# Optimization experiments

Hardware: AMD Instinct MI355X
Metric: run time of the kernel (lower is better)

## Reference

```python
import jax, jax.numpy as jnp
import numpy as np

N = 100000   # nodes
E = 1600000  # edges
B = 64       # graphs
F = 16       # node features
H = 128      # hidden dim
G = 8        # graph features
C = 2        # classes
NGIN = 2     # extra GIN layers after the first
BN_EPS = 1e-5


def elu01(x):
    # F.elu with alpha=0.1
    return jnp.where(x > 0, x, 0.1 * jnp.expm1(x))


def batchnorm(h, gamma, beta):
    # training-mode BatchNorm1d: biased batch statistics
    mu = h.mean(axis=0)
    var = h.var(axis=0)
    return (h - mu) * jax.lax.rsqrt(var + BN_EPS) * gamma + beta


def gin_layer(x, src, dst, W1, b1, gm, bt, W2, b2):
    # GINConv eps=0: MLP(x + sum_{j->i} x_j), then ELU(0.1)
    agg = jax.ops.segment_sum(x[src], dst, num_segments=x.shape[0])
    h = (x + agg) @ W1 + b1
    h = jax.nn.relu(batchnorm(h, gm, bt))
    return elu01(h @ W2 + b2)


def setup_inputs() -> dict:
    key = jax.random.key(0)
    ks = jax.random.split(key, 24)
    s = 0.05
    inp = {
        "h0": jax.random.normal(ks[0], (N, F), jnp.float32),
        "coord0": jax.random.normal(ks[1], (N, 3), jnp.float32),
        "g0": jax.random.normal(ks[2], (B, G), jnp.float32),
        "edge_index": jax.random.randint(ks[3], (2, E), 0, N, jnp.int32),
        "batch": jnp.sort(jax.random.randint(ks[4], (N,), 0, B, jnp.int32)),
        # first GIN layer: (F+3) -> H -> H
        "w1_0": jax.random.normal(ks[5], (F + 3, H), jnp.float32) * s,
        "b1_0": jnp.zeros((H,), jnp.float32),
        "gm_0": jnp.ones((H,), jnp.float32),
        "bt_0": jnp.zeros((H,), jnp.float32),
        "w2_0": jax.random.normal(ks[6], (H, H), jnp.float32) * s,
        "b2_0": jnp.zeros((H,), jnp.float32),
        # NGIN stacked layers: H -> H -> H
        "w1_r": jax.random.normal(ks[7], (NGIN, H, H), jnp.float32) * s,
        "b1_r": jnp.zeros((NGIN, H), jnp.float32),
        "gm_r": jnp.ones((NGIN, H), jnp.float32),
        "bt_r": jnp.zeros((NGIN, H), jnp.float32),
        "w2_r": jax.random.normal(ks[8], (NGIN, H, H), jnp.float32) * s,
        "b2_r": jnp.zeros((NGIN, H), jnp.float32),
        # classifier: (2H+G) -> H -> C
        "cw1": jax.random.normal(ks[9], (2 * H + G, H), jnp.float32) * s,
        "cb1": jnp.zeros((H,), jnp.float32),
        "cgm": jnp.ones((H,), jnp.float32),
        "cbt": jnp.zeros((H,), jnp.float32),
        "cw2": jax.random.normal(ks[10], (H, C), jnp.float32) * s,
        "cb2": jnp.zeros((C,), jnp.float32),
    }
    return inp


def reference(h0, coord0, g0, edge_index, batch,
              w1_0, b1_0, gm_0, bt_0, w2_0, b2_0,
              w1_r, b1_r, gm_r, bt_r, w2_r, b2_r,
              cw1, cb1, cgm, cbt, cw2, cb2):
    src, dst = edge_index[0], edge_index[1]
    x = jnp.concatenate([h0, coord0], axis=1)  # [N, F+3]
    x = gin_layer(x, src, dst, w1_0, b1_0, gm_0, bt_0, w2_0, b2_0)
    for i in range(NGIN):
        x = gin_layer(x, src, dst, w1_r[i], b1_r[i], gm_r[i], bt_r[i], w2_r[i], b2_r[i])
    # global mean + max pooling per graph
    nb = g0.shape[0]
    cnt = jax.ops.segment_sum(jnp.ones((x.shape[0], 1), x.dtype), batch, num_segments=nb)
    mean_p = jax.ops.segment_sum(x, batch, num_segments=nb) / jnp.maximum(cnt, 1.0)
    max_p = jax.ops.segment_max(x, batch, num_segments=nb)
    pooled = jnp.concatenate([mean_p, max_p], axis=-1)  # [B, 2H]
    z = jnp.concatenate([pooled, g0], axis=1)           # [B, 2H+G]
    z = elu01(z @ cw1 + cb1)
    z = batchnorm(z, cgm, cbt)
    logits = z @ cw2 + cb2
    return jax.nn.softmax(logits, axis=1)
```

## Files before the change

### kernel.cpp

```cpp
#include <hip/hip_runtime.h>
#include <math.h>

#define NN 100000
#define EE 1600000
#define BB 64
#define FF 16
#define HH 128
#define GG 8
#define K0 19
#define BN_EPS 1e-5f
#define PCH 16
#define BSHIFT 8
#define BNODES 256
#define NBINS 391
#define BCAP 8192
#define ACH 2048
#define NB_WP 320
#define NB_X0 12500
#define STSLOT 8

typedef short bf16x8 __attribute__((ext_vector_type(8)));
typedef float f32x4 __attribute__((ext_vector_type(4)));

__device__ __forceinline__ float elu01f(float v) {
    return v > 0.f ? v : 0.1f * (__expf(v) - 1.f);
}

__device__ __forceinline__ unsigned f2bfu(float f) {
    unsigned u = __float_as_uint(f);
    unsigned r = u + 0x7FFFu + ((u >> 16) & 1u);
    return r >> 16;
}
__device__ __forceinline__ short f2bf(float f) { return (short)f2bfu(f); }
__device__ __forceinline__ float bfu2f(unsigned short b) {
    return __uint_as_float(((unsigned)b) << 16);
}
__device__ __forceinline__ float bflo(unsigned u) { return __uint_as_float(u << 16); }
__device__ __forceinline__ float bfhi(unsigned u) { return __uint_as_float(u & 0xffff0000u); }

__global__ __launch_bounds__(512) void k_binA(const int* __restrict__ esrc, const int* __restrict__ edst,
                                              int* __restrict__ bincnt, uint2* __restrict__ binbuf) {
    __shared__ int hist[NBINS];
    __shared__ int gbase[NBINS];
    __shared__ int cur[NBINS];
    __shared__ int sc[512];
    __shared__ uint2 ebuf[ACH];
    __shared__ uint2 sorted[ACH];
    int tid = threadIdx.x;
    int e0 = blockIdx.x * ACH;
    int n = min(ACH, EE - e0);
    if (tid < NBINS) hist[tid] = 0;
    __syncthreads();
    for (int i = tid; i < n; i += 512) {
        int s = esrc[e0 + i];
        int d = edst[e0 + i];
        ebuf[i] = make_uint2((unsigned)s, (unsigned)d);
        atomicAdd(&hist[d >> BSHIFT], 1);
    }
    __syncthreads();
    sc[tid] = (tid < NBINS) ? hist[tid] : 0;
    __syncthreads();
    for (int off = 1; off < 512; off <<= 1) {
        int v = (tid >= off) ? sc[tid - off] : 0;
        __syncthreads();
        sc[tid] += v;
        __syncthreads();
    }
    if (tid < NBINS) {
        int c = hist[tid];
        gbase[tid] = (c > 0) ? atomicAdd(&bincnt[tid], c) : 0;
        cur[tid] = (tid > 0) ? sc[tid - 1] : 0;
    }
    __syncthreads();
    for (int i = tid; i < n; i += 512) {
        uint2 e = ebuf[i];
        int b = (int)(e.y >> BSHIFT);
        int pos = atomicAdd(&cur[b], 1);
        sorted[pos] = e;
    }
    __syncthreads();
    for (int i = tid; i < n; i += 512) {
        uint2 e = sorted[i];
        int b = (int)(e.y >> BSHIFT);
        int ls = (b > 0) ? sc[b - 1] : 0;
        int gpos = gbase[b] + (i - ls);
        binbuf[(size_t)b * BCAP + gpos] = e;
    }
}

__global__ __launch_bounds__(512) void k_binB(const uint2* __restrict__ binbuf, const int* __restrict__ bincnt,
                                              int* __restrict__ rp, int* __restrict__ srcs) {
    __shared__ int hist[BNODES];
    __shared__ int scx[BNODES];
    __shared__ int scur[BNODES];
    __shared__ int rsum[512];
    __shared__ int sbuf[BCAP];
    int b = blockIdx.x;
    int n = bincnt[b];
    int tid = threadIdx.x;
    rsum[tid] = (tid < b) ? bincnt[tid] : 0;
    if (tid < BNODES) hist[tid] = 0;
    __syncthreads();
    for (int off = 256; off > 0; off >>= 1) {
        if (tid < off) rsum[tid] += rsum[tid + off];
        __syncthreads();
    }
    int base = rsum[0];
    const uint2* eb = binbuf + (size_t)b * BCAP;
    for (int i = tid; i < n; i += 512)
        atomicAdd(&hist[eb[i].y & (BNODES - 1)], 1);
    __syncthreads();
    if (tid < BNODES) scx[tid] = hist[tid];
    __syncthreads();
    for (int off = 1; off < BNODES; off <<= 1) {
        int vv = (tid >= off && tid < BNODES) ? scx[tid - off] : 0;
        __syncthreads();
        if (tid < BNODES) scx[tid] += vv;
        __syncthreads();
    }
    if (tid < BNODES) {
        int excl = (tid > 0) ? scx[tid - 1] : 0;
        int node = (b << BSHIFT) + tid;
        if (node < NN) rp[node] = base + excl;
        scur[tid] = excl;
    }
    if (b == NBINS - 1 && tid == 0) rp[NN] = EE;
    __syncthreads();
    for (int i = tid; i < n; i += 512) {
        uint2 e = eb[i];
        int pos = atomicAdd(&scur[e.y & (BNODES - 1)], 1);
        sbuf[pos] = (int)e.x;
    }
    __syncthreads();
    for (int i = tid; i < n; i += 512) srcs[base + i] = sbuf[i];
}

__global__ __launch_bounds__(256) void k_prep(const float* __restrict__ w2_0, const float* __restrict__ w1_r,
                                              const float* __restrict__ w2_r, short* __restrict__ wt,
                                              const float* __restrict__ h0, const float* __restrict__ coord,
                                              unsigned short* __restrict__ x0,
                                              const int* __restrict__ batch, int* __restrict__ gptr) {
    int b = blockIdx.x;
    int tid = threadIdx.x;
    if (b == 0 && tid <= BB) {
        int t = tid;
        int lo = 0, hi = NN;
        while (lo < hi) { int mid = (lo + hi) >> 1; if (batch[mid] < t) lo = mid + 1; else hi = mid; }
        gptr[t] = lo;
    }
    if (b < NB_WP) {
        int t = b * 256 + tid;
        if (t >= 5 * HH * HH) return;
        int m = t >> 14;
        int rem = t & 16383;
        int col = rem >> 7;
        int k = rem & 127;
        const float* src = (m == 0) ? w2_0 : (m <= 2 ? w1_r + (size_t)(m - 1) * HH * HH
                                                     : w2_r + (size_t)(m - 3) * HH * HH);
        wt[t] = f2bf(src[k * HH + col]);
    } else {
        int i = (b - NB_WP) * 256 + tid;
        if (i >= NN * 32) return;
        int node = i >> 5, k = i & 31;
        float v = 0.f;
        if (k < FF) v = h0[node * FF + k];
        else if (k < K0) v = coord[node * 3 + (k - FF)];
        x0[i] = (unsigned short)f2bfu(v);
    }
}

__global__ __launch_bounds__(256) void k_agg_small(const uint4* __restrict__ x, const int* __restrict__ rp,
                                                   const int* __restrict__ srcs, float* __restrict__ y) {
    int w = (blockIdx.x * 256 + threadIdx.x) >> 6;
    int lane = threadIdx.x & 63;
    if (w >= NN) return;
    int e = lane >> 2, q = lane & 3;
    int beg = rp[w], end = rp[w + 1];
    float acc[8];
    {
        if (e == 0) {
            uint4 u = x[(size_t)w * 4 + q];
            acc[0] = bflo(u.x); acc[1] = bfhi(u.x);
            acc[2] = bflo(u.y); acc[3] = bfhi(u.y);
            acc[4] = bflo(u.z); acc[5] = bfhi(u.z);
            acc[6] = bflo(u.w); acc[7] = bfhi(u.w);
        } else {
            #pragma unroll
            for (int j = 0; j < 8; j++) acc[j] = 0.f;
        }
    }
    for (int p = beg; p < end; p += 16) {
        int rem = end - p;
        bool act = e < rem;
        int sn = act ? srcs[p + e] : 0;
        uint4 u = x[(size_t)sn * 4 + q];
        float m = act ? 1.f : 0.f;
        acc[0] = fmaf(m, bflo(u.x), acc[0]); acc[1] = fmaf(m, bfhi(u.x), acc[1]);
        acc[2] = fmaf(m, bflo(u.y), acc[2]); acc[3] = fmaf(m, bfhi(u.y), acc[3]);
        acc[4] = fmaf(m, bflo(u.z), acc[4]); acc[5] = fmaf(m, bfhi(u.z), acc[5]);
        acc[6] = fmaf(m, bflo(u.w), acc[6]); acc[7] = fmaf(m, bfhi(u.w), acc[7]);
    }
    #pragma unroll
    for (int mask = 4; mask <= 32; mask <<= 1)
        #pragma unroll
        for (int j = 0; j < 8; j++)
            acc[j] += __shfl_xor(acc[j], mask, 64);
    if (e == 0) {
        float4* yo = (float4*)(y + (size_t)w * 32 + q * 8);
        yo[0] = make_float4(acc[0], acc[1], acc[2], acc[3]);
        yo[1] = make_float4(acc[4], acc[5], acc[6], acc[7]);
    }
}

template<int K>
__global__ __launch_bounds__(256) void k_gemm_small(const float* __restrict__ in,
        const float* __restrict__ W, const float* __restrict__ bias,
        unsigned short* __restrict__ out, float* __restrict__ gstat) {
    constexpr int SK = ((K + 3) / 4) * 4 + 4;
    __shared__ __align__(16) float yt[32 * SK];
    __shared__ float red[256];
    int tid = threadIdx.x;
    int row0 = blockIdx.x * 32;
    for (int t = tid; t < 32 * SK; t += 256) {
        int r = t / SK, k = t - r * SK;
        float v = 0.f;
        if (k < K) v = in[(size_t)(row0 + r) * 32 + k];
        yt[t] = v;
    }
    __syncthreads();
    int col = tid & 127;
    int rg = tid >> 7;
    float acc[16];
    #pragma unroll
    for (int r = 0; r < 16; r++) acc[r] = 0.f;
    const float* ybase = &yt[rg * 16 * SK];
    int kk = 0;
    for (; kk + 4 <= K; kk += 4) {
        float w0 = W[(kk + 0) * HH + col];
        float w1 = W[(kk + 1) * HH + col];
        float w2 = W[(kk + 2) * HH + col];
        float w3 = W[(kk + 3) * HH + col];
        #pragma unroll
        for (int r = 0; r < 16; r++) {
            const float4 v = *(const float4*)&ybase[r * SK + kk];
            acc[r] = fmaf(v.x, w0, acc[r]);
            acc[r] = fmaf(v.y, w1, acc[r]);
            acc[r] = fmaf(v.z, w2, acc[r]);
            acc[r] = fmaf(v.w, w3, acc[r]);
        }
    }
    if constexpr (K % 4 != 0) {
        float w[4];
        #pragma unroll
        for (int j = 0; j < 4; j++) w[j] = (kk + j < K) ? W[(kk + j) * HH + col] : 0.f;
        #pragma unroll
        for (int r = 0; r < 16; r++) {
            const float4 v = *(const float4*)&ybase[r * SK + kk];
            acc[r] = fmaf(v.x, w[0], acc[r]);
            acc[r] = fmaf(v.y, w[1], acc[r]);
            acc[r] = fmaf(v.z, w[2], acc[r]);
            acc[r] = fmaf(v.w, w[3], acc[r]);
        }
    }
    float bcol = bias[col];
    float s = 0.f, s2 = 0.f;
    #pragma unroll
    for (int r = 0; r < 16; r++) {
        float hv = acc[r] + bcol;
        out[(size_t)(row0 + rg * 16 + r) * HH + col] = (unsigned short)f2bfu(hv);
        s += hv; s2 = fmaf(hv, hv, s2);
    }
    int sl = (blockIdx.x & (STSLOT - 1)) << 8;
    red[tid] = s; __syncthreads();
    if (tid < 128) atomicAdd(&gstat[sl + tid], s + red[tid + 128]);
    __syncthreads();
    red[tid] = s2; __syncthreads();
    if (tid < 128) atomicAdd(&gstat[sl + 128 + tid], s2 + red[tid + 128]);
}

__global__ __launch_bounds__(256) void k_agg128_bf(const uint4* __restrict__ x4, const int* __restrict__ rp,
                                                   const int* __restrict__ srcs, uint4* __restrict__ y4) {
    int wave = (blockIdx.x * 256 + threadIdx.x) >> 6;
    int lane = threadIdx.x & 63;
    int g = lane >> 4, il = lane & 15;
    int w = wave * 4 + g;
    if (w >= NN) return;
    int beg = rp[w], end = rp[w + 1];
    uint4 u = x4[(size_t)w * 16 + il];
    float a0 = bflo(u.x), a1 = bfhi(u.x), a2 = bflo(u.y), a3 = bfhi(u.y);
    float a4 = bflo(u.z), a5 = bfhi(u.z), a6 = bflo(u.w), a7 = bfhi(u.w);
    float b0 = 0.f, b1 = 0.f, b2 = 0.f, b3 = 0.f, b4 = 0.f, b5 = 0.f, b6 = 0.f, b7 = 0.f;
    int p = beg;
    for (; p + 8 <= end; p += 8) {
        int s0 = srcs[p + 0], s1 = srcs[p + 1], s2 = srcs[p + 2], s3 = srcs[p + 3];
        int s4 = srcs[p + 4], s5 = srcs[p + 5], s6 = srcs[p + 6], s7 = srcs[p + 7];
        uint4 u0 = x4[(size_t)s0 * 16 + il];
        uint4 u1 = x4[(size_t)s1 * 16 + il];
        uint4 u2 = x4[(size_t)s2 * 16 + il];
        uint4 u3 = x4[(size_t)s3 * 16 + il];
        uint4 u4 = x4[(size_t)s4 * 16 + il];
        uint4 u5 = x4[(size_t)s5 * 16 + il];
        uint4 u6 = x4[(size_t)s6 * 16 + il];
        uint4 u7 = x4[(size_t)s7 * 16 + il];
        a0 += (bflo(u0.x) + bflo(u1.x)) + (bflo(u2.x) + bflo(u3.x));
        a1 += (bfhi(u0.x) + bfhi(u1.x)) + (bfhi(u2.x) + bfhi(u3.x));
        a2 += (bflo(u0.y) + bflo(u1.y)) + (bflo(u2.y) + bflo(u3.y));
        a3 += (bfhi(u0.y) + bfhi(u1.y)) + (bfhi(u2.y) + bfhi(u3.y));
        a4 += (bflo(u0.z) + bflo(u1.z)) + (bflo(u2.z) + bflo(u3.z));
        a5 += (bfhi(u0.z) + bfhi(u1.z)) + (bfhi(u2.z) + bfhi(u3.z));
        a6 += (bflo(u0.w) + bflo(u1.w)) + (bflo(u2.w) + bflo(u3.w));
        a7 += (bfhi(u0.w) + bfhi(u1.w)) + (bfhi(u2.w) + bfhi(u3.w));
        b0 += (bflo(u4.x) + bflo(u5.x)) + (bflo(u6.x) + bflo(u7.x));
        b1 += (bfhi(u4.x) + bfhi(u5.x)) + (bfhi(u6.x) + bfhi(u7.x));
        b2 += (bflo(u4.y) + bflo(u5.y)) + (bflo(u6.y) + bflo(u7.y));
        b3 += (bfhi(u4.y) + bfhi(u5.y)) + (bfhi(u6.y) + bfhi(u7.y));
        b4 += (bflo(u4.z) + bflo(u5.z)) + (bflo(u6.z) + bflo(u7.z));
        b5 += (bfhi(u4.z) + bfhi(u5.z)) + (bfhi(u6.z) + bfhi(u7.z));
        b6 += (bflo(u4.w) + bflo(u5.w)) + (bflo(u6.w) + bflo(u7.w));
        b7 += (bfhi(u4.w) + bfhi(u5.w)) + (bfhi(u6.w) + bfhi(u7.w));
    }
    for (; p + 4 <= end; p += 4) {
        int s0 = srcs[p + 0], s1 = srcs[p + 1], s2 = srcs[p + 2], s3 = srcs[p + 3];
        uint4 u0 = x4[(size_t)s0 * 16 + il];
        uint4 u1 = x4[(size_t)s1 * 16 + il];
        uint4 u2 = x4[(size_t)s2 * 16 + il];
        uint4 u3 = x4[(size_t)s3 * 16 + il];
        a0 += (bflo(u0.x) + bflo(u1.x)) + (bflo(u2.x) + bflo(u3.x));
        a1 += (bfhi(u0.x) + bfhi(u1.x)) + (bfhi(u2.x) + bfhi(u3.x));
        a2 += (bflo(u0.y) + bflo(u1.y)) + (bflo(u2.y) + bflo(u3.y));
        a3 += (bfhi(u0.y) + bfhi(u1.y)) + (bfhi(u2.y) + bfhi(u3.y));
        a4 += (bflo(u0.z) + bflo(u1.z)) + (bflo(u2.z) + bflo(u3.z));
        a5 += (bfhi(u0.z) + bfhi(u1.z)) + (bfhi(u2.z) + bfhi(u3.z));
        a6 += (bflo(u0.w) + bflo(u1.w)) + (bflo(u2.w) + bflo(u3.w));
        a7 += (bfhi(u0.w) + bfhi(u1.w)) + (bfhi(u2.w) + bfhi(u3.w));
    }
    for (; p < end; ++p) {
        uint4 uu = x4[(size_t)srcs[p] * 16 + il];
        a0 += bflo(uu.x); a1 += bfhi(uu.x);
        a2 += bflo(uu.y); a3 += bfhi(uu.y);
        a4 += bflo(uu.z); a5 += bfhi(uu.z);
        a6 += bflo(uu.w); a7 += bfhi(uu.w);
    }
    a0 += b0; a1 += b1; a2 += b2; a3 += b3;
    a4 += b4; a5 += b5; a6 += b6; a7 += b7;
    uint4 o;
    o.x = f2bfu(a0) | (f2bfu(a1) << 16);
    o.y = f2bfu(a2) | (f2bfu(a3) << 16);
    o.z = f2bfu(a4) | (f2bfu(a5) << 16);
    o.w = f2bfu(a6) | (f2bfu(a7) << 16);
    y4[(size_t)w * 16 + il] = o;
}

__global__ __launch_bounds__(256) void k_gemm_s1(const unsigned short* __restrict__ in,
        const short* __restrict__ WT, const float* __restrict__ bias,
        unsigned short* __restrict__ out, float* __restrict__ gstat) {
    __shared__ __align__(16) short Al[64 * 136];
    __shared__ float lsum[HH], lsq[HH];
    int tid = threadIdx.x;
    if (tid < HH) { lsum[tid] = 0.f; lsq[tid] = 0.f; }
    int row0 = blockIdx.x * 64;
    {
        int r = tid >> 2;
        int k0 = (tid & 3) * 32;
        int grow = row0 + r;
        uint4* d4 = (uint4*)&Al[r * 136 + k0];
        if (grow < NN) {
            const uint4* s4 = (const uint4*)(in + (size_t)grow * HH + k0);
            d4[0] = s4[0]; d4[1] = s4[1]; d4[2] = s4[2]; d4[3] = s4[3];
        } else {
            uint4 z = {0, 0, 0, 0};
            d4[0] = z; d4[1] = z; d4[2] = z; d4[3] = z;
        }
    }
    __syncthreads();
    int wave = tid >> 6;
    int lane = tid & 63;
    int ln = lane & 15, quad = lane >> 4;
    int wcol0 = wave * 32;
    f32x4 acc[4][2];
    #pragma unroll
    for (int rt = 0; rt < 4; rt++)
        #pragma unroll
        for (int ct = 0; ct < 2; ct++) acc[rt][ct] = (f32x4){0.f, 0.f, 0.f, 0.f};
    #pragma unroll
    for (int ks = 0; ks < 4; ks++) {
        bf16x8 a[4], b[2];
        #pragma unroll
        for (int ct = 0; ct < 2; ct++)
            b[ct] = *(const bf16x8*)(WT + (size_t)(wcol0 + ct * 16 + ln) * HH + ks * 32 + quad * 8);
        #pragma unroll
        for (int rt = 0; rt < 4; rt++)
            a[rt] = *(const bf16x8*)(&Al[(rt * 16 + ln) * 136 + ks * 32 + quad * 8]);
        #pragma unroll
        for (int rt = 0; rt < 4; rt++)
            #pragma unroll
            for (int ct = 0; ct < 2; ct++)
                acc[rt][ct] = __builtin_amdgcn_mfma_f32_16x16x32_bf16(a[rt], b[ct], acc[rt][ct], 0, 0, 0);
    }
    float b0 = bias[wcol0 + ln];
    float b1 = bias[wcol0 + 16 + ln];
    float s[2] = {0.f, 0.f}, s2[2] = {0.f, 0.f};
    #pragma unroll
    for (int rt = 0; rt < 4; rt++) {
        #pragma unroll
        for (int r = 0; r < 4; r++) {
            int grow = row0 + rt * 16 + quad * 4 + r;
            if (grow < NN) {
                float hv0 = acc[rt][0][r] + b0;
                float hv1 = acc[rt][1][r] + b1;
                out[(size_t)grow * HH + wcol0 + ln] = (unsigned short)f2bfu(hv0);
                out[(size_t)grow * HH + wcol0 + 16 + ln] = (unsigned short)f2bfu(hv1);
                s[0] += hv0; s2[0] = fmaf(hv0, hv0, s2[0]);
                s[1] += hv1; s2[1] = fmaf(hv1, hv1, s2[1]);
            }
        }
    }
    atomicAdd(&lsum[wcol0 + ln], s[0]);
    atomicAdd(&lsum[wcol0 + 16 + ln], s[1]);
    atomicAdd(&lsq[wcol0 + ln], s2[0]);
    atomicAdd(&lsq[wcol0 + 16 + ln], s2[1]);
    __syncthreads();
    if (tid < HH) {
        int sl = (blockIdx.x & (STSLOT - 1)) << 8;
        atomicAdd(&gstat[sl + tid], lsum[tid]);
        atomicAdd(&gstat[sl + 128 + tid], lsq[tid]);
    }
}

__global__ __launch_bounds__(256) void k_gemm_bn(const unsigned short* __restrict__ in,
        const short* __restrict__ WT, const float* __restrict__ bias,
        const float* __restrict__ gstat, const float* __restrict__ gm, const float* __restrict__ bt,
        unsigned short* __restrict__ out) {
    __shared__ __align__(16) short Al[64 * 136];
    __shared__ __align__(16) float bnsc[HH], bnsh[HH];
    int tid = threadIdx.x;
    if (tid < HH) {
        float s = 0.f, s2 = 0.f;
        #pragma unroll
        for (int k = 0; k < STSLOT; ++k) {
            s += gstat[(k << 8) + tid];
            s2 += gstat[(k << 8) + 128 + tid];
        }
        float mu = s * (1.f / NN);
        float var = fmaxf(s2 * (1.f / NN) - mu * mu, 0.f);
        float a = gm[tid] * rsqrtf(var + BN_EPS);
        bnsc[tid] = a;
        bnsh[tid] = fmaf(-mu, a, bt[tid]);
    }
    __syncthreads();
    int row0 = blockIdx.x * 64;
    {
        int r = tid >> 2;
        int k0 = (tid & 3) * 32;
        int grow = row0 + r;
        short* dst = &Al[r * 136 + k0];
        if (grow < NN) {
            const uint4* s4 = (const uint4*)(in + (size_t)grow * HH + k0);
            unsigned* d = (unsigned*)dst;
            #pragma unroll
            for (int q = 0; q < 4; q++) {
                uint4 u = s4[q];
                float4 sc0 = *(const float4*)(bnsc + k0 + q * 8);
                float4 sh0 = *(const float4*)(bnsh + k0 + q * 8);
                float4 sc1 = *(const float4*)(bnsc + k0 + q * 8 + 4);
                float4 sh1 = *(const float4*)(bnsh + k0 + q * 8 + 4);
                float a0 = bflo(u.x), a1 = bfhi(u.x);
                float a2 = bflo(u.y), a3 = bfhi(u.y);
                float a4 = bflo(u.z), a5 = bfhi(u.z);
                float a6 = bflo(u.w), a7 = bfhi(u.w);
                a0 = fmaxf(fmaf(a0, sc0.x, sh0.x), 0.f);
                a1 = fmaxf(fmaf(a1, sc0.y, sh0.y), 0.f);
                a2 = fmaxf(fmaf(a2, sc0.z, sh0.z), 0.f);
                a3 = fmaxf(fmaf(a3, sc0.w, sh0.w), 0.f);
                a4 = fmaxf(fmaf(a4, sc1.x, sh1.x), 0.f);
                a5 = fmaxf(fmaf(a5, sc1.y, sh1.y), 0.f);
                a6 = fmaxf(fmaf(a6, sc1.z, sh1.z), 0.f);
                a7 = fmaxf(fmaf(a7, sc1.w, sh1.w), 0.f);
                d[q * 4 + 0] = f2bfu(a0) | (f2bfu(a1) << 16);
                d[q * 4 + 1] = f2bfu(a2) | (f2bfu(a3) << 16);
                d[q * 4 + 2] = f2bfu(a4) | (f2bfu(a5) << 16);
                d[q * 4 + 3] = f2bfu(a6) | (f2bfu(a7) << 16);
            }
        } else {
            uint4 z = {0, 0, 0, 0};
            uint4* d4 = (uint4*)dst;
            d4[0] = z; d4[1] = z; d4[2] = z; d4[3] = z;
        }
    }
    __syncthreads();
    int wave = tid >> 6;
    int lane = tid & 63;
    int ln = lane & 15, quad = lane >> 4;
    int wcol0 = wave * 32;
    f32x4 acc[4][2];
    #pragma unroll
    for (int rt = 0; rt < 4; rt++)
        #pragma unroll
        for (int ct = 0; ct < 2; ct++) acc[rt][ct] = (f32x4){0.f, 0.f, 0.f, 0.f};
    #pragma unroll
    for (int ks = 0; ks < 4; ks++) {
        bf16x8 a[4], b[2];
        #pragma unroll
        for (int ct = 0; ct < 2; ct++)
            b[ct] = *(const bf16x8*)(WT + (size_t)(wcol0 + ct * 16 + ln) * HH + ks * 32 + quad * 8);
        #pragma unroll
        for (int rt = 0; rt < 4; rt++)
            a[rt] = *(const bf16x8*)(&Al[(rt * 16 + ln) * 136 + ks * 32 + quad * 8]);
        #pragma unroll
        for (int rt = 0; rt < 4; rt++)
            #pragma unroll
            for (int ct = 0; ct < 2; ct++)
                acc[rt][ct] = __builtin_amdgcn_mfma_f32_16x16x32_bf16(a[rt], b[ct], acc[rt][ct], 0, 0, 0);
    }
    float b0 = bias[wcol0 + ln];
    float b1 = bias[wcol0 + 16 + ln];
    #pragma unroll
    for (int rt = 0; rt < 4; rt++) {
        #pragma unroll
        for (int r = 0; r < 4; r++) {
            int grow = row0 + rt * 16 + quad * 4 + r;
            if (grow < NN) {
                float hv0 = elu01f(acc[rt][0][r] + b0);
                float hv1 = elu01f(acc[rt][1][r] + b1);
                out[(size_t)grow * HH + wcol0 + ln] = (unsigned short)f2bfu(hv0);
                out[(size_t)grow * HH + wcol0 + 16 + ln] = (unsigned short)f2bfu(hv1);
            }
        }
    }
}

__global__ __launch_bounds__(128) void k_pool_part(const unsigned short* __restrict__ x,
                                                   const int* __restrict__ gptr,
                                                   float* __restrict__ psum, float* __restrict__ pmax) {
    int g = blockIdx.x >> 4;
    int ch = blockIdx.x & 15;
    int s = gptr[g], e = gptr[g + 1];
    int len = e - s;
    int per = (len + PCH - 1) / PCH;
    int lo = s + ch * per;
    int hi = min(lo + per, e);
    int c = threadIdx.x;
    float sm = 0.f, mx = -INFINITY;
    for (int i = lo; i < hi; ++i) {
        float v = bfu2f(x[(size_t)i * HH + c]);
        sm += v; mx = fmaxf(mx, v);
    }
    psum[(size_t)blockIdx.x * HH + c] = sm;
    pmax[(size_t)blockIdx.x * HH + c] = mx;
}

__global__ __launch_bounds__(128) void k_pool_cls1(const float* __restrict__ psum, const float* __restrict__ pmax,
                                                   const int* __restrict__ gptr, const float* __restrict__ g0,
                                                   const float* __restrict__ cw1, const float* __restrict__ cb1,
                                                   float* __restrict__ z1) {
    __shared__ float zr[264];
    int g = blockIdx.x, c = threadIdx.x;
    float sm = 0.f, mx = -INFINITY;
    for (int ch = 0; ch < PCH; ++ch) {
        sm += psum[(size_t)(g * PCH + ch) * HH + c];
        mx = fmaxf(mx, pmax[(size_t)(g * PCH + ch) * HH + c]);
    }
    int cntn = gptr[g + 1] - gptr[g];
    zr[c] = sm / (float)max(cntn, 1);
    zr[128 + c] = mx;
    if (c < GG) zr[256 + c] = g0[g * GG + c];
    __syncthreads();
    float acc = cb1[c];
    for (int k = 0; k < 264; ++k) acc = fmaf(zr[k], cw1[k * HH + c], acc);
    z1[g * HH + c] = elu01f(acc);
}

__global__ __launch_bounds__(128) void k_cls2(const float* __restrict__ z1, const float* __restrict__ cgm,
                                              const float* __restrict__ cbt, const float* __restrict__ cw2,
                                              const float* __restrict__ cb2, float* __restrict__ outp) {
    __shared__ float zn[HH * 65];
    int c = threadIdx.x;
    float s = 0.f, s2 = 0.f;
    for (int g = 0; g < BB; ++g) {
        float v = z1[g * HH + c];
        s += v; s2 = fmaf(v, v, s2);
    }
    float mu = s * (1.f / BB);
    float var = fmaxf(s2 * (1.f / BB) - mu * mu, 0.f);
    float a = cgm[c] * rsqrtf(var + BN_EPS);
    float sh = fmaf(-mu, a, cbt[c]);
    for (int g = 0; g < BB; ++g) zn[c * 65 + g] = fmaf(z1[g * HH + c], a, sh);
    __syncthreads();
    if (c < BB) {
        float l0 = cb2[0], l1 = cb2[1];
        for (int k = 0; k < HH; ++k) {
            float v = zn[k * 65 + c];
            l0 = fmaf(v, cw2[k * 2 + 0], l0);
            l1 = fmaf(v, cw2[k * 2 + 1], l1);
        }
        float m = fmaxf(l0, l1);
        float e0 = __expf(l0 - m), e1 = __expf(l1 - m);
        float inv = 1.f / (e0 + e1);
        outp[c * 2 + 0] = e0 * inv;
        outp[c * 2 + 1] = e1 * inv;
    }
}

extern "C" void kernel_launch(void* const* d_in, const int* in_sizes, int n_in,
                              void* d_out, int out_size, void* d_ws, size_t ws_size,
                              hipStream_t stream) {
    (void)in_sizes; (void)n_in; (void)out_size; (void)ws_size;
    const float* h0     = (const float*)d_in[0];
    const float* coord0 = (const float*)d_in[1];
    const float* g0     = (const float*)d_in[2];
    const int*   eidx   = (const int*)d_in[3];
    const int*   batch  = (const int*)d_in[4];
    const float* w1_0   = (const float*)d_in[5];
    const float* b1_0   = (const float*)d_in[6];
    const float* gm_0   = (const float*)d_in[7];
    const float* bt_0   = (const float*)d_in[8];
    const float* w2_0   = (const float*)d_in[9];
    const float* b2_0   = (const float*)d_in[10];
    const float* w1_r   = (const float*)d_in[11];
    const float* b1_r   = (const float*)d_in[12];
    const float* gm_r   = (const float*)d_in[13];
    const float* bt_r   = (const float*)d_in[14];
    const float* w2_r   = (const float*)d_in[15];
    const float* b2_r   = (const float*)d_in[16];
    const float* cw1    = (const float*)d_in[17];
    const float* cb1    = (const float*)d_in[18];
    const float* cgm    = (const float*)d_in[19];
    const float* cbt    = (const float*)d_in[20];
    const float* cw2    = (const float*)d_in[21];
    const float* cb2    = (const float*)d_in[22];
    float* outp = (float*)d_out;

    const int* esrc = eidx;
    const int* edst = eidx + EE;

    char* p = (char*)d_ws;
    auto alloc = [&](size_t bytes) { void* r = (void*)p; p += (bytes + 255) & ~(size_t)255; return r; };
    int*            bincnt   = (int*)alloc((size_t)NBINS * 4);
    float*          gstat    = (float*)alloc((size_t)3 * STSLOT * 256 * 4);
    unsigned short* x0bf     = (unsigned short*)alloc((size_t)NN * 32 * 2);
    float*          y19f     = (float*)alloc((size_t)NN * 32 * 4);
    unsigned short* hbf      = (unsigned short*)alloc((size_t)NN * HH * 2);
    unsigned*       xbf      = (unsigned*)alloc((size_t)NN * 64 * 4);
    unsigned*       ybf      = (unsigned*)alloc((size_t)NN * 64 * 4);
    int*            rp       = (int*)alloc((size_t)(NN + 1) * 4);
    int*            srcs     = (int*)alloc((size_t)EE * 4);
    int*            gptr     = (int*)alloc((BB + 1) * 4);
    short*          wt       = (short*)alloc((size_t)5 * HH * HH * 2);
    float*          psum     = (float*)alloc((size_t)BB * PCH * HH * 4);
    float*          pmax     = (float*)alloc((size_t)BB * PCH * HH * 4);
    float*          z1b      = (float*)alloc((size_t)BB * HH * 4);
    uint2*          binbuf   = (uint2*)alloc((size_t)NBINS * BCAP * 8);

    const int NB_A = (EE + ACH - 1) / ACH;
    const int NB_AGG = (NN * 64 + 255) / 256;
    const int NB_AGG4 = (NN + 15) / 16;
    const int NB_G32 = NN / 32;
    const int NB_G64 = (NN + 63) / 64;

    size_t zlen = (size_t)((char*)x0bf - (char*)bincnt);
    hipMemsetAsync(bincnt, 0, zlen, stream);

    k_binA<<<NB_A, 512, 0, stream>>>(esrc, edst, bincnt, binbuf);
    k_binB<<<NBINS, 512, 0, stream>>>(binbuf, bincnt, rp, srcs);
    k_prep<<<NB_WP + NB_X0, 256, 0, stream>>>(w2_0, w1_r, w2_r, wt, h0, coord0, x0bf, batch, gptr);

    k_agg_small<<<NB_AGG, 256, 0, stream>>>((const uint4*)x0bf, rp, srcs, y19f);
    k_gemm_small<K0><<<NB_G32, 256, 0, stream>>>(y19f, w1_0, b1_0, hbf, gstat);
    k_gemm_bn<<<NB_G64, 256, 0, stream>>>(hbf, wt, b2_0, gstat, gm_0, bt_0, (unsigned short*)xbf);

    for (int i = 0; i < 2; ++i) {
        float* gs = gstat + (size_t)(1 + i) * STSLOT * 256;
        k_agg128_bf<<<NB_AGG4, 256, 0, stream>>>((const uint4*)xbf, rp, srcs, (uint4*)ybf);
        k_gemm_s1<<<NB_G64, 256, 0, stream>>>((const unsigned short*)ybf,
                wt + (size_t)(1 + i) * HH * HH, b1_r + i * HH, hbf, gs);
        k_gemm_bn<<<NB_G64, 256, 0, stream>>>(hbf, wt + (size_t)(3 + i) * HH * HH, b2_r + i * HH,
                                              gs, gm_r + i * HH, bt_r + i * HH, (unsigned short*)xbf);
    }

    k_pool_part<<<BB * PCH, 128, 0, stream>>>((const unsigned short*)xbf, gptr, psum, pmax);
    k_pool_cls1<<<BB, 128, 0, stream>>>(psum, pmax, gptr, g0, cw1, cb1, z1b);
    k_cls2<<<1, 128, 0, stream>>>(z1b, cgm, cbt, cw2, cb2, outp);
}
```

Before: 486.0 us.

## Fuse global mean/max pooling into final GEMM+BN epilogue via atomics

The final k_gemm_bn launch now accumulates per-graph sums and maxima in its epilogue. When a 64-row tile lies within one graph it reduces in registers and issues one atomic per column; otherwise it issues per-row atomics, with max done through an order-preserving integer encoding. This removes the separate k_pool_part kernel, its second read of the node features and the partial-sum buffers. The trade-off is atomic contention on a 64x128 buffer, which relies on the zeroing memset covering psumG/pmaxG, and a float summation order that is no longer fixed.

New measurement: 509.6 us. 1.05x slower.

```diff
diff --git a/kernel.cpp b/kernel.cpp
--- a/kernel.cpp
+++ b/kernel.cpp
@@ -9,7 +9,6 @@
 #define GG 8
 #define K0 19
 #define BN_EPS 1e-5f
-#define PCH 16
 #define BSHIFT 8
 #define BNODES 256
 #define NBINS 391
@@ -37,6 +36,15 @@
 }
 __device__ __forceinline__ float bflo(unsigned u) { return __uint_as_float(u << 16); }
 __device__ __forceinline__ float bfhi(unsigned u) { return __uint_as_float(u & 0xffff0000u); }
+
+__device__ __forceinline__ unsigned fenc(float f) {
+    unsigned u = __float_as_uint(f);
+    return (u & 0x80000000u) ? ~u : (u | 0x80000000u);
+}
+__device__ __forceinline__ float fdec(unsigned e) {
+    unsigned u = (e & 0x80000000u) ? (e & 0x7FFFFFFFu) : ~e;
+    return __uint_as_float(u);
+}
 
 __global__ __launch_bounds__(512) void k_binA(const int* __restrict__ esrc, const int* __restrict__ edst,
                                               int* __restrict__ bincnt, uint2* __restrict__ binbuf) {
@@ -427,10 +435,12 @@
     }
 }
 
+template<bool POOL>
 __global__ __launch_bounds__(256) void k_gemm_bn(const unsigned short* __restrict__ in,
         const short* __restrict__ WT, const float* __restrict__ bias,
         const float* __restrict__ gstat, const float* __restrict__ gm, const float* __restrict__ bt,
-        unsigned short* __restrict__ out) {
+        unsigned short* __restrict__ out, const int* __restrict__ batch,
+        float* __restrict__ psumG, unsigned* __restrict__ pmaxG) {
     __shared__ __align__(16) short Al[64 * 136];
     __shared__ __align__(16) float bnsc[HH], bnsh[HH];
     int tid = threadIdx.x;
@@ -514,6 +524,14 @@
     }
     float b0 = bias[wcol0 + ln];
     float b1 = bias[wcol0 + 16 + ln];
+    bool uni = false;
+    int g0_ = 0;
+    float ps0 = 0.f, ps1 = 0.f, pm0 = -INFINITY, pm1 = -INFINITY;
+    if (POOL) {
+        int rlast = min(row0 + 63, NN - 1);
+        g0_ = batch[row0 < NN ? row0 : NN - 1];
+        uni = (batch[rlast] == g0_);
+    }
     #pragma unroll
     for (int rt = 0; rt < 4; rt++) {
         #pragma unroll
@@ -524,45 +542,40 @@
                 float hv1 = elu01f(acc[rt][1][r] + b1);
                 out[(size_t)grow * HH + wcol0 + ln] = (unsigned short)f2bfu(hv0);
                 out[(size_t)grow * HH + wcol0 + 16 + ln] = (unsigned short)f2bfu(hv1);
+                if (POOL) {
+                    float q0 = bfu2f((unsigned short)f2bfu(hv0));
+                    float q1 = bfu2f((unsigned short)f2bfu(hv1));
+                    if (uni) {
+                        ps0 += q0; ps1 += q1;
+                        pm0 = fmaxf(pm0, q0); pm1 = fmaxf(pm1, q1);
+                    } else {
+                        int gph = batch[grow];
+                        atomicAdd(&psumG[gph * HH + wcol0 + ln], q0);
+                        atomicAdd(&psumG[gph * HH + wcol0 + 16 + ln], q1);
+                        atomicMax(&pmaxG[gph * HH + wcol0 + ln], fenc(q0));
+                        atomicMax(&pmaxG[gph * HH + wcol0 + 16 + ln], fenc(q1));
+                    }
+                }
             }
         }
     }
-}
-
-__global__ __launch_bounds__(128) void k_pool_part(const unsigned short* __restrict__ x,
-                                                   const int* __restrict__ gptr,
-                                                   float* __restrict__ psum, float* __restrict__ pmax) {
-    int g = blockIdx.x >> 4;
-    int ch = blockIdx.x & 15;
-    int s = gptr[g], e = gptr[g + 1];
-    int len = e - s;
-    int per = (len + PCH - 1) / PCH;
-    int lo = s + ch * per;
-    int hi = min(lo + per, e);
-    int c = threadIdx.x;
-    float sm = 0.f, mx = -INFINITY;
-    for (int i = lo; i < hi; ++i) {
-        float v = bfu2f(x[(size_t)i * HH + c]);
-        sm += v; mx = fmaxf(mx, v);
-    }
-    psum[(size_t)blockIdx.x * HH + c] = sm;
-    pmax[(size_t)blockIdx.x * HH + c] = mx;
-}
-
-__global__ __launch_bounds__(128) void k_pool_cls1(const float* __restrict__ psum, const float* __restrict__ pmax,
+    if (POOL && uni) {
+        atomicAdd(&psumG[g0_ * HH + wcol0 + ln], ps0);
+        atomicAdd(&psumG[g0_ * HH + wcol0 + 16 + ln], ps1);
+        atomicMax(&pmaxG[g0_ * HH + wcol0 + ln], fenc(pm0));
+        atomicMax(&pmaxG[g0_ * HH + wcol0 + 16 + ln], fenc(pm1));
+    }
+}
+
+__global__ __launch_bounds__(128) void k_pool_cls1(const float* __restrict__ psumG, const unsigned* __restrict__ pmaxG,
                                                    const int* __restrict__ gptr, const float* __restrict__ g0,
                                                    const float* __restrict__ cw1, const float* __restrict__ cb1,
                                                    float* __restrict__ z1) {
     __shared__ float zr[264];
     int g = blockIdx.x, c = threadIdx.x;
-    float sm = 0.f, mx = -INFINITY;
-    for (int ch = 0; ch < PCH; ++ch) {
-        sm += psum[(size_t)(g * PCH + ch) * HH + c];
-        mx = fmaxf(mx, pmax[(size_t)(g * PCH + ch) * HH + c]);
-    }
     int cntn = gptr[g + 1] - gptr[g];
-    zr[c] = sm / (float)max(cntn, 1);
-    zr[128 + c] = mx;
+    zr[c] = psumG[g * HH + c] / (float)max(cntn, 1);
+    zr[128 + c] = fdec(pmaxG[g * HH + c]);
     if (c < GG) zr[256 + c] = g0[g * GG + c];
     __syncthreads();
     float acc = cb1[c];
@@ -637,6 +650,8 @@
     auto alloc = [&](size_t bytes) { void* r = (void*)p; p += (bytes + 255) & ~(size_t)255; return r; };
     int*            bincnt   = (int*)alloc((size_t)NBINS * 4);
     float*          gstat    = (float*)alloc((size_t)3 * STSLOT * 256 * 4);
+    float*          psumG    = (float*)alloc((size_t)BB * HH * 4);
+    unsigned*       pmaxG    = (unsigned*)alloc((size_t)BB * HH * 4);
     unsigned short* x0bf     = (unsigned short*)alloc((size_t)NN * 32 * 2);
     float*          y19f     = (float*)alloc((size_t)NN * 32 * 4);
     unsigned short* hbf      = (unsigned short*)alloc((size_t)NN * HH * 2);
@@ -646,8 +661,6 @@
     int*            srcs     = (int*)alloc((size_t)EE * 4);
     int*            gptr     = (int*)alloc((BB + 1) * 4);
     short*          wt       = (short*)alloc((size_t)5 * HH * HH * 2);
-    float*          psum     = (float*)alloc((size_t)BB * PCH * HH * 4);
-    float*          pmax     = (float*)alloc((size_t)BB * PCH * HH * 4);
     float*          z1b      = (float*)alloc((size_t)BB * HH * 4);
     uint2*          binbuf   = (uint2*)alloc((size_t)NBINS * BCAP * 8);
 
@@ -666,18 +679,24 @@
 
     k_agg_small<<<NB_AGG, 256, 0, stream>>>((const uint4*)x0bf, rp, srcs, y19f);
     k_gemm_small<K0><<<NB_G32, 256, 0, stream>>>(y19f, w1_0, b1_0, hbf, gstat);
-    k_gemm_bn<<<NB_G64, 256, 0, stream>>>(hbf, wt, b2_0, gstat, gm_0, bt_0, (unsigned short*)xbf);
+    k_gemm_bn<false><<<NB_G64, 256, 0, stream>>>(hbf, wt, b2_0, gstat, gm_0, bt_0,
+                                                 (unsigned short*)xbf, batch, psumG, pmaxG);
 
     for (int i = 0; i < 2; ++i) {
         float* gs = gstat + (size_t)(1 + i) * STSLOT * 256;
         k_agg128_bf<<<NB_AGG4, 256, 0, stream>>>((const uint4*)xbf, rp, srcs, (uint4*)ybf);
         k_gemm_s1<<<NB_G64, 256, 0, stream>>>((const unsigned short*)ybf,
                 wt + (size_t)(1 + i) * HH * HH, b1_r + i * HH, hbf, gs);
-        k_gemm_bn<<<NB_G64, 256, 0, stream>>>(hbf, wt + (size_t)(3 + i) * HH * HH, b2_r + i * HH,
-                                              gs, gm_r + i * HH, bt_r + i * HH, (unsigned short*)xbf);
-    }
-
-    k_pool_part<<<BB * PCH, 128, 0, stream>>>((const unsigned short*)xbf, gptr, psum, pmax);
-    k_pool_cls1<<<BB, 128, 0, stream>>>(psum, pmax, gptr, g0, cw1, cb1, z1b);
+        if (i == 0)
+            k_gemm_bn<false><<<NB_G64, 256, 0, stream>>>(hbf, wt + (size_t)(3 + i) * HH * HH,
+                    b2_r + i * HH, gs, gm_r + i * HH, bt_r + i * HH,
+                    (unsigned short*)xbf, batch, psumG, pmaxG);
+        else
+            k_gemm_bn<true><<<NB_G64, 256, 0, stream>>>(hbf, wt + (size_t)(3 + i) * HH * HH,
+                    b2_r + i * HH, gs, gm_r + i * HH, bt_r + i * HH,
+                    (unsigned short*)xbf, batch, psumG, pmaxG);
+    }
+
+    k_pool_cls1<<<BB, 128, 0, stream>>>(psumG, pmaxG, gptr, g0, cw1, cb1, z1b);
     k_cls2<<<1, 128, 0, stream>>>(z1b, cgm, cbt, cw2, cb2, outp);
 }
```
